# Performance work log

Hardware: AMD Instinct MI355X
Metric: run time of the kernel (lower is better)

## Reference

```python
import jax, jax.numpy as jnp
import numpy as np

D_MODEL = 2048
N_HEADS = 16
DIM_K = 128
DIM_V = 128
D_MID = 6144
STD = 0.02


def setup_inputs() -> dict:
    key = jax.random.key(0)
    k_x, k_wq, k_wo, k_K, k_V = jax.random.split(key, 5)
    B, T = 2, 2048
    x = jax.random.normal(k_x, (B, T, D_MODEL), dtype=jnp.float32)
    # nn.Linear weights: stored as (out, in); we keep jax convention (in, out)
    Wq = jax.random.normal(k_wq, (D_MODEL, N_HEADS * DIM_K), dtype=jnp.float32) * (1.0 / np.sqrt(D_MODEL))
    Wo = jax.random.normal(k_wo, (N_HEADS * DIM_V, D_MODEL), dtype=jnp.float32) * (1.0 / np.sqrt(N_HEADS * DIM_V))
    K = jax.random.normal(k_K, (N_HEADS, D_MID, DIM_K), dtype=jnp.float32) * STD
    V = jax.random.normal(k_V, (N_HEADS, D_MID, DIM_V), dtype=jnp.float32) * STD
    return {"x": x, "Wq": Wq, "Wo": Wo, "K": K, "V": V}


def reference(x, Wq, Wo, K, V):
    B, T, _ = x.shape
    # Q projection: (b,t,d) @ (d, h*dk) -> (b,t,h,dk)
    Q = (x @ Wq).reshape(B, T, N_HEADS, DIM_K)
    # per-head GEMM 1: (b,t,h,dk) x (h,m,dk) -> (b,t,h,m)
    scores = jnp.einsum('bthk,hmk->bthm', Q, K)
    scores = jax.nn.silu(scores)
    # per-head GEMM 2: (b,t,h,m) x (h,m,dv) -> (b,t,h,dv)
    out = jnp.einsum('bthm,hmv->bthv', scores, V)
    out = out.reshape(B, T, N_HEADS * DIM_V)
    return out @ Wo
```

## Files before the change

### kernel.cpp

```cpp
#include <hip/hip_runtime.h>

typedef unsigned short ushort_t;
typedef __attribute__((ext_vector_type(8))) short bf16x8;
typedef __attribute__((ext_vector_type(4))) float f32x4;

__device__ __forceinline__ unsigned short f2b(float f) {
  unsigned u = __builtin_bit_cast(unsigned, f);
  u += 0x7fffu + ((u >> 16) & 1u);
  return (unsigned short)(u >> 16);
}

__device__ __forceinline__ void gload_lds16(const ushort_t* g, ushort_t* l) {
  auto* gp = (const __attribute__((address_space(1))) ushort_t*)g;
  auto* lp = (__attribute__((address_space(3))) ushort_t*)l;
  __builtin_amdgcn_global_load_lds(gp, lp, 16, 0, 0);
}

__device__ __forceinline__ void storeC(float* C, size_t i, float v) { C[i] = v; }
__device__ __forceinline__ void storeC(ushort_t* C, size_t i, float v) { C[i] = f2b(v); }


__global__ __launch_bounds__(256) void cast_f32_bf16_k(const float4* __restrict__ in,
                                                       ushort4* __restrict__ out, int n4) {
  int i = blockIdx.x * 256 + threadIdx.x;
  if (i < n4) {
    float4 v = in[i];
    ushort4 o;
    o.x = f2b(v.x); o.y = f2b(v.y); o.z = f2b(v.z); o.w = f2b(v.w);
    out[i] = o;
  }
}

__global__ __launch_bounds__(256) void transpose_cast_k(const float* __restrict__ in,
                                                        ushort_t* __restrict__ out,
                                                        int rows, int cols) {
  __shared__ float tile[64][65];
  size_t boff = (size_t)blockIdx.z * rows * cols;
  const float* inb = in + boff;
  ushort_t* outb = out + boff;
  int r0 = blockIdx.y * 64, c0 = blockIdx.x * 64;
  int lr = threadIdx.x >> 6, lc = threadIdx.x & 63;
#pragma unroll
  for (int i = 0; i < 16; i++) {
    int r = i * 4 + lr;
    tile[r][lc] = inb[(size_t)(r0 + r) * cols + (c0 + lc)];
  }
  __syncthreads();
#pragma unroll
  for (int i = 0; i < 16; i++) {
    int oc = i * 4 + lr;
    outb[(size_t)(c0 + oc) * rows + (r0 + lc)] = f2b(tile[lc][oc]);
  }
}


template <typename OutT>
__global__ __launch_bounds__(256) void gemm_bt_k(const ushort_t* __restrict__ A,
                                                 const ushort_t* __restrict__ BT,
                                                 OutT* __restrict__ C, int M, int N, int K) {
  __shared__ alignas(16) ushort_t lA[128 * 32];
  __shared__ alignas(16) ushort_t lB[128 * 32];
  int tid = threadIdx.x, lane = tid & 63, wave = tid >> 6;
  int wm = wave >> 1, wn = wave & 1;
  int m0 = blockIdx.y * 128, n0 = blockIdx.x * 128;
  int lr = lane & 15, lk = lane >> 4;
  f32x4 acc[4][4] = {};
  for (int k0 = 0; k0 < K; k0 += 32) {
    __syncthreads();
#pragma unroll
    for (int t = 0; t < 2; t++) {
      int cb = wave * 128 + t * 64;
      int c = cb + lane;
      int r = c >> 2;
      int kc = (c & 3) ^ ((r >> 1) & 3);
      gload_lds16(A + (size_t)(m0 + r) * K + k0 + kc * 8, lA + (size_t)cb * 8);
      gload_lds16(BT + (size_t)(n0 + r) * K + k0 + kc * 8, lB + (size_t)cb * 8);
    }
    __syncthreads();
    bf16x8 aF[4], bF[4];
#pragma unroll
    for (int i = 0; i < 4; i++) {
      int r = wm * 64 + i * 16 + lr;
      int kc = lk ^ ((r >> 1) & 3);
      aF[i] = *(const bf16x8*)(lA + r * 32 + kc * 8);
    }
#pragma unroll
    for (int j = 0; j < 4; j++) {
      int r = wn * 64 + j * 16 + lr;
      int kc = lk ^ ((r >> 1) & 3);
      bF[j] = *(const bf16x8*)(lB + r * 32 + kc * 8);
    }
#pragma unroll
    for (int i = 0; i < 4; i++)
#pragma unroll
      for (int j = 0; j < 4; j++)
        acc[i][j] = __builtin_amdgcn_mfma_f32_16x16x32_bf16(aF[i], bF[j], acc[i][j], 0, 0, 0);
  }
#pragma unroll
  for (int i = 0; i < 4; i++) {
#pragma unroll
    for (int j = 0; j < 4; j++) {
      int row = m0 + wm * 64 + i * 16 + lk * 4;
      int col = n0 + wn * 64 + j * 16 + lr;
#pragma unroll
      for (int r = 0; r < 4; r++) storeC(C, (size_t)(row + r) * N + col, acc[i][j][r]);
    }
  }
}


__global__ __launch_bounds__(256) void fused_mid_k(const ushort_t* __restrict__ Qb,
                                                   const ushort_t* __restrict__ Kb,
                                                   const ushort_t* __restrict__ VTb,
                                                   ushort_t* __restrict__ mid) {
  __shared__ alignas(16) ushort_t lQ[128 * 128];
  __shared__ alignas(16) ushort_t lK[64 * 128];
  __shared__ alignas(16) ushort_t lV[128 * 64];
  __shared__ alignas(16) ushort_t lS[128 * 64];
  int tid = threadIdx.x, lane = tid & 63, wave = tid >> 6;
  int wm = wave >> 1, wn = wave & 1;
  int lr = lane & 15, lk = lane >> 4;
  int t0 = blockIdx.x * 128;
  int h = blockIdx.y;
  const ushort_t* Qh = Qb + (size_t)t0 * 2048 + h * 128;
  const ushort_t* Kh = Kb + (size_t)h * 6144 * 128;
  const ushort_t* Vh = VTb + (size_t)h * 128 * 6144;

#pragma unroll
  for (int t = 0; t < 8; t++) {
    int cb = (wave * 8 + t) * 64;
    int c = cb + lane;
    int r = c >> 4;
    int kc = (c & 15) ^ (r & 15);
    gload_lds16(Qh + (size_t)r * 2048 + kc * 8, lQ + (size_t)cb * 8);
  }

  f32x4 acc[4][4] = {};
  for (int m0 = 0; m0 < 6144; m0 += 64) {
    __syncthreads();
#pragma unroll
    for (int t = 0; t < 4; t++) {
      int cb = (wave * 4 + t) * 64;
      int c = cb + lane;
      int rk = c >> 4;
      int kck = (c & 15) ^ (rk & 15);
      gload_lds16(Kh + (size_t)(m0 + rk) * 128 + kck * 8, lK + (size_t)cb * 8);
      int rv = c >> 3;
      int kcv = (c & 7) ^ (rv & 7);
      gload_lds16(Vh + (size_t)rv * 6144 + m0 + kcv * 8, lV + (size_t)cb * 8);
    }
    __syncthreads();
    f32x4 s[4][2] = {};
#pragma unroll
    for (int ks = 0; ks < 4; ks++) {
      bf16x8 qF[4], kF[2];
#pragma unroll
      for (int i = 0; i < 4; i++) {
        int r = wm * 64 + i * 16 + lr;
        int kc = (ks * 4 + lk) ^ (r & 15);
        qF[i] = *(const bf16x8*)(lQ + r * 128 + kc * 8);
      }
#pragma unroll
      for (int j = 0; j < 2; j++) {
        int r = wn * 32 + j * 16 + lr;
        int kc = (ks * 4 + lk) ^ (r & 15);
        kF[j] = *(const bf16x8*)(lK + r * 128 + kc * 8);
      }
#pragma unroll
      for (int i = 0; i < 4; i++)
#pragma unroll
        for (int j = 0; j < 2; j++)
          s[i][j] = __builtin_amdgcn_mfma_f32_16x16x32_bf16(qF[i], kF[j], s[i][j], 0, 0, 0);
    }
#pragma unroll
    for (int i = 0; i < 4; i++) {
#pragma unroll
      for (int j = 0; j < 2; j++) {
        int mcol = wn * 32 + j * 16 + lr;
#pragma unroll
        for (int r = 0; r < 4; r++) {
          int trow = wm * 64 + i * 16 + lk * 4 + r;
          float x = s[i][j][r];
          float sg = __builtin_amdgcn_rcpf(1.0f + __expf(-x));
          int mc = (mcol >> 3) ^ (trow & 7);
          lS[trow * 64 + mc * 8 + (mcol & 7)] = f2b(x * sg);
        }
      }
    }
    __syncthreads();
#pragma unroll
    for (int ks = 0; ks < 2; ks++) {
      bf16x8 sF[4], vF[4];
#pragma unroll
      for (int i = 0; i < 4; i++) {
        int r = wm * 64 + i * 16 + lr;
        int kc = (ks * 4 + lk) ^ (r & 7);
        sF[i] = *(const bf16x8*)(lS + r * 64 + kc * 8);
      }
#pragma unroll
      for (int j = 0; j < 4; j++) {
        int r = wn * 64 + j * 16 + lr;
        int kc = (ks * 4 + lk) ^ (r & 7);
        vF[j] = *(const bf16x8*)(lV + r * 64 + kc * 8);
      }
#pragma unroll
      for (int i = 0; i < 4; i++)
#pragma unroll
        for (int j = 0; j < 4; j++)
          acc[i][j] = __builtin_amdgcn_mfma_f32_16x16x32_bf16(sF[i], vF[j], acc[i][j], 0, 0, 0);
    }
  }
#pragma unroll
  for (int i = 0; i < 4; i++) {
#pragma unroll
    for (int j = 0; j < 4; j++) {
      int row = t0 + wm * 64 + i * 16 + lk * 4;
      int col = h * 128 + wn * 64 + j * 16 + lr;
#pragma unroll
      for (int r = 0; r < 4; r++) mid[(size_t)(row + r) * 2048 + col] = f2b(acc[i][j][r]);
    }
  }
}


extern "C" void kernel_launch(void* const* d_in, const int* in_sizes, int n_in,
                              void* d_out, int out_size, void* d_ws, size_t ws_size,
                              hipStream_t stream) {
  const float* x  = (const float*)d_in[0];
  const float* Wq = (const float*)d_in[1];
  const float* Wo = (const float*)d_in[2];
  const float* K  = (const float*)d_in[3];
  const float* V  = (const float*)d_in[4];
  float* out = (float*)d_out;

  ushort_t* xb   = (ushort_t*)d_ws;
  ushort_t* WqT  = xb + 8388608;
  ushort_t* WoT  = WqT + 4194304;
  ushort_t* Kb   = WoT + 4194304;
  ushort_t* VTb  = Kb + 12582912;
  ushort_t* Qb   = VTb + 12582912;
  ushort_t* midb = xb;

  cast_f32_bf16_k<<<8192, 256, 0, stream>>>((const float4*)x, (ushort4*)xb, 2097152);
  cast_f32_bf16_k<<<12288, 256, 0, stream>>>((const float4*)K, (ushort4*)Kb, 3145728);
  transpose_cast_k<<<dim3(32, 32, 1), 256, 0, stream>>>(Wq, WqT, 2048, 2048);
  transpose_cast_k<<<dim3(32, 32, 1), 256, 0, stream>>>(Wo, WoT, 2048, 2048);
  transpose_cast_k<<<dim3(2, 96, 16), 256, 0, stream>>>(V, VTb, 6144, 128);

  gemm_bt_k<ushort_t><<<dim3(16, 32), 256, 0, stream>>>(xb, WqT, Qb, 4096, 2048, 2048);
  fused_mid_k<<<dim3(32, 16), 256, 0, stream>>>(Qb, Kb, VTb, midb);
  gemm_bt_k<float><<<dim3(16, 32), 256, 0, stream>>>(midb, WoT, out, 4096, 2048, 2048);
}
```

Measured before the change: 435.9 us.

## Double-buffer K/V tiles, keep Q in registers, remap blocks across heads

```diff
diff --git a/kernel.cpp b/kernel.cpp
--- a/kernel.cpp
+++ b/kernel.cpp
@@ -3,11 +3,17 @@
 typedef unsigned short ushort_t;
 typedef __attribute__((ext_vector_type(8))) short bf16x8;
 typedef __attribute__((ext_vector_type(4))) float f32x4;
+typedef __attribute__((ext_vector_type(2))) unsigned int u32x2;
 
 __device__ __forceinline__ unsigned short f2b(float f) {
   unsigned u = __builtin_bit_cast(unsigned, f);
   u += 0x7fffu + ((u >> 16) & 1u);
   return (unsigned short)(u >> 16);
+}
+
+__device__ __forceinline__ float silu_f(float x) {
+  float e = __builtin_amdgcn_exp2f(x * -1.44269504f);
+  return x * __builtin_amdgcn_rcpf(1.0f + e);
 }
 
 __device__ __forceinline__ void gload_lds16(const ushort_t* g, ushort_t* l) {
@@ -113,81 +119,85 @@
                                                    const ushort_t* __restrict__ Kb,
                                                    const ushort_t* __restrict__ VTb,
                                                    ushort_t* __restrict__ mid) {
-  __shared__ alignas(16) ushort_t lQ[128 * 128];
-  __shared__ alignas(16) ushort_t lK[64 * 128];
-  __shared__ alignas(16) ushort_t lV[128 * 64];
+  __shared__ alignas(16) ushort_t lK[2][64 * 128];
+  __shared__ alignas(16) ushort_t lV[2][128 * 64];
   __shared__ alignas(16) ushort_t lS[128 * 64];
   int tid = threadIdx.x, lane = tid & 63, wave = tid >> 6;
   int wm = wave >> 1, wn = wave & 1;
   int lr = lane & 15, lk = lane >> 4;
-  int t0 = blockIdx.x * 128;
-  int h = blockIdx.y;
+  int id = blockIdx.x;
+  int h = (id & 7) * 2 + (id >> 8);
+  int t0 = ((id >> 3) & 31) * 128;
   const ushort_t* Qh = Qb + (size_t)t0 * 2048 + h * 128;
   const ushort_t* Kh = Kb + (size_t)h * 6144 * 128;
   const ushort_t* Vh = VTb + (size_t)h * 128 * 6144;
 
-#pragma unroll
-  for (int t = 0; t < 8; t++) {
-    int cb = (wave * 8 + t) * 64;
-    int c = cb + lane;
-    int r = c >> 4;
-    int kc = (c & 15) ^ (r & 15);
-    gload_lds16(Qh + (size_t)r * 2048 + kc * 8, lQ + (size_t)cb * 8);
-  }
+  bf16x8 qF[4][4];
+#pragma unroll
+  for (int i = 0; i < 4; i++)
+#pragma unroll
+    for (int ks = 0; ks < 4; ks++)
+      qF[i][ks] = *(const bf16x8*)(Qh + (size_t)(wm * 64 + i * 16 + lr) * 2048 + ks * 32 + lk * 8);
+
+#define STAGE(B, M0)                                                              \
+  {                                                                               \
+    _Pragma("unroll") for (int t = 0; t < 4; t++) {                               \
+      int cb = (wave * 4 + t) * 64;                                               \
+      int c = cb + lane;                                                          \
+      int rk = c >> 4;                                                            \
+      int kck = (c & 15) ^ (rk & 15);                                             \
+      gload_lds16(Kh + (size_t)((M0) + rk) * 128 + kck * 8, lK[B] + (size_t)cb * 8); \
+      int rv = c >> 3;                                                            \
+      int kcv = (c & 7) ^ (rv & 7);                                               \
+      gload_lds16(Vh + (size_t)rv * 6144 + (M0) + kcv * 8, lV[B] + (size_t)cb * 8);  \
+    }                                                                             \
+  }
+
+  STAGE(0, 0);
 
   f32x4 acc[4][4] = {};
-  for (int m0 = 0; m0 < 6144; m0 += 64) {
-    __syncthreads();
-#pragma unroll
-    for (int t = 0; t < 4; t++) {
-      int cb = (wave * 4 + t) * 64;
-      int c = cb + lane;
-      int rk = c >> 4;
-      int kck = (c & 15) ^ (rk & 15);
-      gload_lds16(Kh + (size_t)(m0 + rk) * 128 + kck * 8, lK + (size_t)cb * 8);
-      int rv = c >> 3;
-      int kcv = (c & 7) ^ (rv & 7);
-      gload_lds16(Vh + (size_t)rv * 6144 + m0 + kcv * 8, lV + (size_t)cb * 8);
-    }
-    __syncthreads();
-    f32x4 s[4][2] = {};
+  int cur = 0;
+  for (int m0 = 0; m0 < 6144; m0 += 64, cur ^= 1) {
+    asm volatile("s_waitcnt vmcnt(0)" ::: "memory");
+    __builtin_amdgcn_s_barrier();
+    asm volatile("" ::: "memory");
+    if (m0 + 64 < 6144) STAGE(cur ^ 1, m0 + 64);
+
+    f32x4 s2[2][4] = {};
 #pragma unroll
     for (int ks = 0; ks < 4; ks++) {
-      bf16x8 qF[4], kF[2];
-#pragma unroll
-      for (int i = 0; i < 4; i++) {
-        int r = wm * 64 + i * 16 + lr;
-        int kc = (ks * 4 + lk) ^ (r & 15);
-        qF[i] = *(const bf16x8*)(lQ + r * 128 + kc * 8);
-      }
+      bf16x8 kF[2];
 #pragma unroll
       for (int j = 0; j < 2; j++) {
         int r = wn * 32 + j * 16 + lr;
         int kc = (ks * 4 + lk) ^ (r & 15);
-        kF[j] = *(const bf16x8*)(lK + r * 128 + kc * 8);
-      }
-#pragma unroll
-      for (int i = 0; i < 4; i++)
-#pragma unroll
-        for (int j = 0; j < 2; j++)
-          s[i][j] = __builtin_amdgcn_mfma_f32_16x16x32_bf16(qF[i], kF[j], s[i][j], 0, 0, 0);
-    }
-#pragma unroll
-    for (int i = 0; i < 4; i++) {
-#pragma unroll
-      for (int j = 0; j < 2; j++) {
-        int mcol = wn * 32 + j * 16 + lr;
-#pragma unroll
-        for (int r = 0; r < 4; r++) {
-          int trow = wm * 64 + i * 16 + lk * 4 + r;
-          float x = s[i][j][r];
-          float sg = __builtin_amdgcn_rcpf(1.0f + __expf(-x));
-          int mc = (mcol >> 3) ^ (trow & 7);
-          lS[trow * 64 + mc * 8 + (mcol & 7)] = f2b(x * sg);
-        }
-      }
-    }
-    __syncthreads();
+        kF[j] = *(const bf16x8*)(lK[cur] + r * 128 + kc * 8);
+      }
+#pragma unroll
+      for (int j = 0; j < 2; j++)
+#pragma unroll
+        for (int i = 0; i < 4; i++)
+          s2[j][i] = __builtin_amdgcn_mfma_f32_16x16x32_bf16(kF[j], qF[i][ks], s2[j][i], 0, 0, 0);
+    }
+#pragma unroll
+    for (int j = 0; j < 2; j++) {
+#pragma unroll
+      for (int i = 0; i < 4; i++) {
+        int mb = wn * 32 + j * 16 + lk * 4;
+        int t = wm * 64 + i * 16 + lr;
+        float v0 = silu_f(s2[j][i][0]), v1 = silu_f(s2[j][i][1]);
+        float v2 = silu_f(s2[j][i][2]), v3 = silu_f(s2[j][i][3]);
+        unsigned d0, d1;
+        asm("v_cvt_pk_bf16_f32 %0, %1, %2" : "=v"(d0) : "v"(v0), "v"(v1));
+        asm("v_cvt_pk_bf16_f32 %0, %1, %2" : "=v"(d1) : "v"(v2), "v"(v3));
+        int mc = (mb >> 3) ^ (t & 7);
+        u32x2 val; val.x = d0; val.y = d1;
+        *(u32x2*)(lS + t * 64 + mc * 8 + (mb & 7)) = val;
+      }
+    }
+    asm volatile("s_waitcnt lgkmcnt(0)" ::: "memory");
+    __builtin_amdgcn_s_barrier();
+    asm volatile("" ::: "memory");
 #pragma unroll
     for (int ks = 0; ks < 2; ks++) {
       bf16x8 sF[4], vF[4];
@@ -201,7 +211,7 @@
       for (int j = 0; j < 4; j++) {
         int r = wn * 64 + j * 16 + lr;
         int kc = (ks * 4 + lk) ^ (r & 7);
-        vF[j] = *(const bf16x8*)(lV + r * 64 + kc * 8);
+        vF[j] = *(const bf16x8*)(lV[cur] + r * 64 + kc * 8);
       }
 #pragma unroll
       for (int i = 0; i < 4; i++)
@@ -210,6 +220,7 @@
           acc[i][j] = __builtin_amdgcn_mfma_f32_16x16x32_bf16(sF[i], vF[j], acc[i][j], 0, 0, 0);
     }
   }
+#undef STAGE
 #pragma unroll
   for (int i = 0; i < 4; i++) {
 #pragma unroll
@@ -248,6 +259,6 @@
   transpose_cast_k<<<dim3(2, 96, 16), 256, 0, stream>>>(V, VTb, 6144, 128);
 
   gemm_bt_k<ushort_t><<<dim3(16, 32), 256, 0, stream>>>(xb, WqT, Qb, 4096, 2048, 2048);
-  fused_mid_k<<<dim3(32, 16), 256, 0, stream>>>(Qb, Kb, VTb, midb);
+  fused_mid_k<<<512, 256, 0, stream>>>(Qb, Kb, VTb, midb);
   gemm_bt_k<float><<<dim3(16, 32), 256, 0, stream>>>(midb, WoT, out, 4096, 2048, 2048);
 }
```

Result: faster. 418.4 us (-4.0%).
